# Optimization experiments

Hardware: AMD Instinct MI355X
Metric: run time of the kernel (lower is better)

## Reference

```python
import jax, jax.numpy as jnp
import numpy as np
from jax import lax

N = 100_000          # points
NEIGH = 16           # max_num_neighbors
E = N * NEIGH        # edges
DIN = 128            # num_inputs
D2 = 64              # bottleneck dim = num_outputs // 4
DOUT = 256           # num_outputs
K = 15               # num_kernel_points
SIGMA = 0.04         # kernel_influence_dist = prev_grid_size * sigma
NEG = 0.1            # LeakyReLU slope
EPS = 1e-5           # BatchNorm eps


def leaky(x):
    return jnp.where(x >= 0, x, NEG * x)


def batchnorm(x, g, b):
    # training-mode BN over the point dimension (biased variance, like torch)
    m = jnp.mean(x, axis=0)
    v = jnp.var(x, axis=0)
    return (x - m) * (g / jnp.sqrt(v + EPS)) + b


def setup_inputs() -> dict:
    key = jax.random.key(0)
    ks = jax.random.split(key, 12)
    pos = jax.random.uniform(ks[0], (N, 4), dtype=jnp.float32) * 0.1  # col 0: batch idx (unused, non-strided)
    x = jax.random.normal(ks[1], (N, DIN), dtype=jnp.float32)
    e_ref = jax.random.randint(ks[2], (E,), 0, N)
    e_query = jax.random.randint(ks[3], (E,), 0, N)
    # fixed kernel point positions within the influence radius
    kernel_points = jax.random.normal(ks[4], (K, 3), dtype=jnp.float32) * (0.5 * SIGMA)
    W1 = jax.random.normal(ks[5], (DIN, D2), dtype=jnp.float32) / np.sqrt(DIN)
    W_kp = jax.random.normal(ks[6], (K, D2, D2), dtype=jnp.float32) / np.sqrt(D2 * K)
    W2 = jax.random.normal(ks[7], (D2, DOUT), dtype=jnp.float32) / np.sqrt(D2)
    Wsc = jax.random.normal(ks[8], (DIN, DOUT), dtype=jnp.float32) / np.sqrt(DIN)
    ones = lambda d: jnp.ones((d,), jnp.float32)
    zeros = lambda d: jnp.zeros((d,), jnp.float32)
    return dict(pos=pos, x=x, e_ref=e_ref, e_query=e_query,
                W1=W1, g1=ones(D2), b1=zeros(D2),
                kernel_points=kernel_points, W_kp=W_kp, gkp=ones(D2), bkp=zeros(D2),
                W2=W2, g2=ones(DOUT), b2=zeros(DOUT),
                Wsc=Wsc, gsc=ones(DOUT), bsc=zeros(DOUT))


def reference(pos, x, e_ref, e_query, W1, g1, b1, kernel_points, W_kp, gkp, bkp,
              W2, g2, b2, Wsc, gsc, bsc):
    n = x.shape[0]
    # bottleneck unary_1: Linear(no bias) -> BN -> LeakyReLU
    h = leaky(batchnorm(x @ W1, g1, b1))                      # [N, D2]
    # KPConv (rigid, linear influence, 'sum' aggregation); non-strided: query_pos == pos
    rel = pos[e_ref, 1:] - pos[e_query, 1:]                    # [E, 3]
    d2 = jnp.sum((rel[:, None, :] - kernel_points[None]) ** 2, axis=-1)  # [E, K]
    infl = jnp.maximum(0.0, 1.0 - jnp.sqrt(d2) / SIGMA)        # [E, K]
    feat_e = h[e_ref]                                          # [E, D2] neighbor gather

    def body(acc, inp):
        infl_k, Wk = inp                                       # [E], [D2, D2]
        agg = jax.ops.segment_sum(infl_k[:, None] * feat_e, e_query, num_segments=n)
        return acc + agg @ Wk, None

    y0 = jnp.zeros((n, W_kp.shape[-1]), x.dtype)
    y, _ = lax.scan(body, y0, (infl.T, W_kp))                  # [N, D2]
    # SimpleBlock post: BN -> LeakyReLU
    y = leaky(batchnorm(y, gkp, bkp))
    # bottleneck unary_2: Linear -> BN -> LeakyReLU
    y = leaky(batchnorm(y @ W2, g2, b2))
    # shortcut (num_inputs != num_outputs): Linear -> BN, no activation; residual add
    skip = batchnorm(x @ Wsc, gsc, bsc)
    return y + skip
```

## Files before the change

### kernel.cpp

```cpp
#include <hip/hip_runtime.h>
#include <math.h>

#define NP   100000
#define EDG  1600000
#define NK   15
#define SIGK 0.04f
#define SCH  2048
#define SNB  49
#define MAXE 384
#define AGP  968

typedef __bf16 v8bf __attribute__((ext_vector_type(8)));
typedef __bf16 bf4  __attribute__((ext_vector_type(4)));
typedef float  v4f  __attribute__((ext_vector_type(4)));

__device__ __forceinline__ float lk(float v) { return v >= 0.f ? v : 0.1f * v; }
__device__ __forceinline__ float bf2f(__bf16 b) { return (float)b; }

template <int KIN, int NB, bool TRANS, bool OUTBF>
__global__ __launch_bounds__(256) void mgemm_k(const float* __restrict__ X,
                                               const __bf16* __restrict__ Wp,
                                               void* __restrict__ Out, int n, int Ntot,
                                               const float* __restrict__ ta,
                                               const float* __restrict__ tb,
                                               float* __restrict__ osum,
                                               float* __restrict__ osq) {
  constexpr int PITCH = KIN + 8;
  constexpr int NT = NB / 16;
  __shared__ __bf16 al[128 * PITCH];
  __shared__ float red[2][NB][4];
  const int tid = threadIdx.x;
  const int r0 = blockIdx.x << 7;
  const int nb0 = blockIdx.y * NB;

  constexpr int QKS = (KIN == 128) ? 5 : 4;
  for (int idx = tid; idx < (128 << QKS); idx += 256) {
    const int r = idx >> QKS, q = (idx & ((1 << QKS) - 1)) << 2;
    const int row = r0 + r;
    float4 v = make_float4(0.f, 0.f, 0.f, 0.f);
    if (row < n) {
      v = *(const float4*)&X[(size_t)row * KIN + q];
      if (TRANS) {
        v.x = lk(ta[q + 0] * v.x + tb[q + 0]);
        v.y = lk(ta[q + 1] * v.y + tb[q + 1]);
        v.z = lk(ta[q + 2] * v.z + tb[q + 2]);
        v.w = lk(ta[q + 3] * v.w + tb[q + 3]);
      }
    }
    bf4 o;
    o[0] = (__bf16)v.x; o[1] = (__bf16)v.y; o[2] = (__bf16)v.z; o[3] = (__bf16)v.w;
    *(bf4*)&al[r * PITCH + q] = o;
  }
  __syncthreads();

  const int wv = tid >> 6, lane = tid & 63;
  const int mr = lane & 15, quad = lane >> 4;
  const int ntg0 = nb0 >> 4;
  const int NTG = Ntot >> 4;
  v4f acc[2][NT];
#pragma unroll
  for (int a = 0; a < 2; ++a)
#pragma unroll
    for (int b = 0; b < NT; ++b) acc[a][b] = (v4f){0.f, 0.f, 0.f, 0.f};

#pragma unroll
  for (int ks = 0; ks < KIN / 32; ++ks) {
    v8bf bf[NT];
#pragma unroll
    for (int nt = 0; nt < NT; ++nt)
      bf[nt] = ((const v8bf*)Wp)[((size_t)ks * NTG + ntg0 + nt) * 64 + lane];
#pragma unroll
    for (int mt = 0; mt < 2; ++mt) {
      const int row = (wv << 5) + (mt << 4) + mr;
      const v8bf av = *(const v8bf*)&al[row * PITCH + (ks << 5) + (quad << 3)];
#pragma unroll
      for (int nt = 0; nt < NT; ++nt)
        acc[mt][nt] = __builtin_amdgcn_mfma_f32_16x16x32_bf16(av, bf[nt], acc[mt][nt], 0, 0, 0);
    }
  }

  float csum[NT], csq[NT];
#pragma unroll
  for (int nt = 0; nt < NT; ++nt) { csum[nt] = 0.f; csq[nt] = 0.f; }
#pragma unroll
  for (int mt = 0; mt < 2; ++mt)
#pragma unroll
    for (int nt = 0; nt < NT; ++nt)
#pragma unroll
      for (int r = 0; r < 4; ++r) {
        const float v = acc[mt][nt][r];
        const int row = r0 + (wv << 5) + (mt << 4) + (quad << 2) + r;
        if (row < n) {
          const size_t o = (size_t)row * Ntot + nb0 + (nt << 4) + mr;
          if (OUTBF) ((__bf16*)Out)[o] = (__bf16)v;
          else       ((float*)Out)[o] = v;
        }
        csum[nt] += v;
        csq[nt] += v * v;
      }
#pragma unroll
  for (int nt = 0; nt < NT; ++nt) {
    float s = csum[nt], q = csq[nt];
    s += __shfl_down(s, 32); s += __shfl_down(s, 16);
    q += __shfl_down(q, 32); q += __shfl_down(q, 16);
    if (quad == 0) { red[0][(nt << 4) + mr][wv] = s; red[1][(nt << 4) + mr][wv] = q; }
  }
  __syncthreads();
  if (tid < NB) {
    const float s = red[0][tid][0] + red[0][tid][1] + red[0][tid][2] + red[0][tid][3];
    const float q = red[1][tid][0] + red[1][tid][1] + red[1][tid][2] + red[1][tid][3];
    const int rep = (blockIdx.x & 31) * Ntot;
    atomicAdd(&osum[rep + nb0 + tid], s);
    atomicAdd(&osq[rep + nb0 + tid], q);
  }
}

__global__ void finalize_k(const float* __restrict__ sum, const float* __restrict__ sq,
                           const float* __restrict__ g, const float* __restrict__ b,
                           float* __restrict__ oa, float* __restrict__ ob, int C, int R,
                           float invn) {
  const int c = threadIdx.x;
  if (c < C) {
    float s = 0.f, q = 0.f;
    for (int r = 0; r < R; ++r) { s += sum[r * C + c]; q += sq[r * C + c]; }
    const float m = s * invn;
    const float var = q * invn - m * m;
    const float a = g[c] / sqrtf(var + 1e-5f);
    oa[c] = a;
    ob[c] = b[c] - m * a;
  }
}

__global__ __launch_bounds__(256) void normleaky_k(const __bf16* __restrict__ t,
                                                   __bf16* __restrict__ hb,
                                                   const float* __restrict__ a,
                                                   const float* __restrict__ b) {
  const int idx = (blockIdx.x << 8) + threadIdx.x;
  const int c = (idx << 2) & 63;
  const bf4 v = *(const bf4*)&t[(size_t)idx << 2];
  bf4 o;
  o[0] = (__bf16)lk(a[c + 0] * bf2f(v[0]) + b[c + 0]);
  o[1] = (__bf16)lk(a[c + 1] * bf2f(v[1]) + b[c + 1]);
  o[2] = (__bf16)lk(a[c + 2] * bf2f(v[2]) + b[c + 2]);
  o[3] = (__bf16)lk(a[c + 3] * bf2f(v[3]) + b[c + 3]);
  *(bf4*)&hb[(size_t)idx << 2] = o;
}

__global__ __launch_bounds__(256) void final_k(float* __restrict__ o,
                                               const __bf16* __restrict__ t2,
                                               const __bf16* __restrict__ tsc,
                                               const float* __restrict__ a2,
                                               const float* __restrict__ b2,
                                               const float* __restrict__ asc,
                                               const float* __restrict__ bsc) {
  const int idx = (blockIdx.x << 8) + threadIdx.x;
  const int c = (idx << 2) & 255;
  const bf4 tv = *(const bf4*)&t2[(size_t)idx << 2];
  const bf4 sv = *(const bf4*)&tsc[(size_t)idx << 2];
  float4 r;
  r.x = lk(a2[c + 0] * bf2f(tv[0]) + b2[c + 0]) + asc[c + 0] * bf2f(sv[0]) + bsc[c + 0];
  r.y = lk(a2[c + 1] * bf2f(tv[1]) + b2[c + 1]) + asc[c + 1] * bf2f(sv[1]) + bsc[c + 1];
  r.z = lk(a2[c + 2] * bf2f(tv[2]) + b2[c + 2]) + asc[c + 2] * bf2f(sv[2]) + bsc[c + 2];
  r.w = lk(a2[c + 3] * bf2f(tv[3]) + b2[c + 3]) + asc[c + 3] * bf2f(sv[3]) + bsc[c + 3];
  ((float4*)o)[idx] = r;
}

__device__ __forceinline__ bool edge_active(const float* __restrict__ pos,
                                            const float* __restrict__ kp,
                                            int ref, int q) {
  const float4 pr = *(const float4*)&pos[ref * 4];
  const float4 pq = *(const float4*)&pos[q * 4];
  const float rx = pr.y - pq.y, ry = pr.z - pq.z, rz = pr.w - pq.w;
  bool act = false;
#pragma unroll
  for (int k = 0; k < NK; ++k) {
    const float dx = rx - kp[k * 3 + 0];
    const float dy = ry - kp[k * 3 + 1];
    const float dz = rz - kp[k * 3 + 2];
    act = act || (dx * dx + dy * dy + dz * dz < SIGK * SIGK);
  }
  return act;
}

__global__ __launch_bounds__(256) void hist_k(const int* __restrict__ er,
                                              const int* __restrict__ eq,
                                              const float* __restrict__ pos,
                                              const float* __restrict__ kp,
                                              int* __restrict__ cnt,
                                              unsigned char* __restrict__ flags) {
  const int stride = gridDim.x << 8;
  for (int e = (blockIdx.x << 8) + threadIdx.x; e < EDG; e += stride) {
    const int q = eq[e];
    const bool act = edge_active(pos, kp, er[e], q);
    flags[e] = act ? 1 : 0;
    if (act) atomicAdd(&cnt[q], 1);
  }
}

__global__ __launch_bounds__(256) void scanA_k(const int* __restrict__ cnt, int* __restrict__ part) {
  __shared__ int s[256];
  const int tid = threadIdx.x;
  const int base = blockIdx.x * SCH;
  int acc = 0;
  for (int i = tid; i < SCH; i += 256) {
    const int idx = base + i;
    if (idx < NP) acc += cnt[idx];
  }
  s[tid] = acc;
  __syncthreads();
  for (int d = 128; d > 0; d >>= 1) {
    if (tid < d) s[tid] += s[tid + d];
    __syncthreads();
  }
  if (tid == 0) part[blockIdx.x] = s[0];
}

__global__ void scanB_k(int* __restrict__ part, int* __restrict__ off) {
  if (threadIdx.x == 0) {
    int run = 0;
    for (int i = 0; i < SNB; ++i) { const int v = part[i]; part[i] = run; run += v; }
    off[NP] = run;
  }
}

__global__ __launch_bounds__(256) void scanC_k(const int* __restrict__ cnt,
                                               const int* __restrict__ part,
                                               int* __restrict__ off, int* __restrict__ cur) {
  __shared__ int s[256];
  const int tid = threadIdx.x;
  const int base = blockIdx.x * SCH + tid * 8;
  int loc[8];
  int mysum = 0;
#pragma unroll
  for (int j = 0; j < 8; ++j) {
    const int idx = base + j;
    const int v = (idx < NP) ? cnt[idx] : 0;
    loc[j] = mysum;
    mysum += v;
  }
  s[tid] = mysum;
  __syncthreads();
  for (int d = 1; d < 256; d <<= 1) {
    int v = (tid >= d) ? s[tid - d] : 0;
    __syncthreads();
    s[tid] += v;
    __syncthreads();
  }
  const int tb = part[blockIdx.x] + s[tid] - mysum;
#pragma unroll
  for (int j = 0; j < 8; ++j) {
    const int idx = base + j;
    if (idx < NP) { off[idx] = tb + loc[j]; cur[idx] = tb + loc[j]; }
  }
}

__global__ __launch_bounds__(256) void scat_k(const int* __restrict__ er,
                                              const int* __restrict__ eq,
                                              const unsigned char* __restrict__ flags,
                                              int* __restrict__ cur, int* __restrict__ sref) {
  const int stride = gridDim.x << 8;
  for (int e = (blockIdx.x << 8) + threadIdx.x; e < EDG; e += stride) {
    if (flags[e]) {
      const int p = atomicAdd(&cur[eq[e]], 1);
      if (p < EDG) sref[p] = er[e];
    }
  }
}

__device__ __forceinline__ void wshuf1(const float* W, __bf16* Wp, int idx, int Ntot) {
  const int j = idx & 7;
  const int lane = (idx >> 3) & 63;
  const int rest = idx >> 9;
  const int NTG = Ntot >> 4;
  const int ntg = rest % NTG;
  const int ks = rest / NTG;
  Wp[idx] = (__bf16)W[(size_t)(ks * 32 + ((lane >> 4) << 3) + j) * Ntot + ntg * 16 + (lane & 15)];
}

__global__ __launch_bounds__(256) void allshuf_k(const float* __restrict__ W1,
                                                 const float* __restrict__ Wsc,
                                                 const float* __restrict__ W2,
                                                 const float* __restrict__ Wkp,
                                                 __bf16* __restrict__ base) {
  const int i = (blockIdx.x << 8) + threadIdx.x;
  if (i < 8192) {
    wshuf1(W1, base, i, 64);
  } else if (i < 40960) {
    wshuf1(Wsc, base + 8192, i - 8192, 256);
  } else if (i < 57344) {
    wshuf1(W2, base + 40960, i - 40960, 256);
  } else if (i < 118784) {
    const int idx = i - 57344;
    const int j = idx & 7;
    const int lane = (idx >> 3) & 63;
    const int nt = (idx >> 9) & 3;
    const int kb = (idx >> 11) & 1;
    const int k = idx >> 12;
    const int kd = kb * 32 + ((lane >> 4) << 3) + j;
    const int n = nt * 16 + (lane & 15);
    (base + 57344)[idx] = (__bf16)Wkp[(k * 64 + kd) * 64 + n];
  }
}

__global__ __launch_bounds__(256, 4) void kpagg_k(const float* __restrict__ pos,
                                                  const int* __restrict__ sref,
                                                  const int* __restrict__ off,
                                                  const float* __restrict__ kpts,
                                                  const __bf16* __restrict__ Wf,
                                                  const __bf16* __restrict__ hb,
                                                  float* __restrict__ y,
                                                  float* __restrict__ osum,
                                                  float* __restrict__ osq) {
  constexpr int INFL_BYTES = MAXE * 16 * 4;
  constexpr int UNION_BYTES = 16 * AGP * 2;
  __shared__ __align__(16) char uSm[UNION_BYTES];
  __shared__ int qoffL[17];
  __shared__ float kpL[48];
  float* inflF = (float*)uSm;
  int* refsL = (int*)(uSm + INFL_BYTES);
  __bf16* aggL = (__bf16*)uSm;

  const int tid = threadIdx.x;
  const int q0 = blockIdx.x << 4;
  if (tid < 17) qoffL[tid] = off[q0 + tid];
  if (tid >= 32 && tid < 32 + 45) kpL[tid - 32] = kpts[tid - 32];
  __syncthreads();

  const int e0 = qoffL[0];
  int nE = qoffL[16] - e0;
  if (nE > MAXE) nE = MAXE;
  if (nE == 0 && tid == 0) refsL[0] = 0;

  for (int i = tid; i < nE; i += 256) {
    const int e = e0 + i;
    const int ref = sref[e];
    refsL[i] = ref;
    int lo = 0, hi = 16;
    while (hi - lo > 1) { const int mid = (lo + hi) >> 1; if (qoffL[mid] <= e) lo = mid; else hi = mid; }
    const int q = q0 + lo;
    const float4 pr = *(const float4*)&pos[ref * 4];
    const float4 pq = *(const float4*)&pos[q * 4];
    const float rx = pr.y - pq.y, ry = pr.z - pq.z, rz = pr.w - pq.w;
    float wk[16];
#pragma unroll
    for (int k = 0; k < NK; ++k) {
      const float dx = rx - kpL[k * 3 + 0];
      const float dy = ry - kpL[k * 3 + 1];
      const float dz = rz - kpL[k * 3 + 2];
      const float w = 1.f - sqrtf(dx * dx + dy * dy + dz * dz) * (1.f / SIGK);
      wk[k] = w > 0.f ? w : 0.f;
    }
    wk[15] = 0.f;
    *(float4*)&inflF[i * 16 + 0]  = make_float4(wk[0], wk[1], wk[2], wk[3]);
    *(float4*)&inflF[i * 16 + 4]  = make_float4(wk[4], wk[5], wk[6], wk[7]);
    *(float4*)&inflF[i * 16 + 8]  = make_float4(wk[8], wk[9], wk[10], wk[11]);
    *(float4*)&inflF[i * 16 + 12] = make_float4(wk[12], wk[13], wk[14], wk[15]);
  }
  __syncthreads();

  const int wv = tid >> 6, lane = tid & 63;
  const int ql = (wv << 2) + (lane >> 4);
  const int t4 = (lane & 15) << 2;
  const int le0 = qoffL[ql] - e0;
  int le1 = qoffL[ql + 1] - e0;
  if (le1 > nE) le1 = nE;
  const int len = le1 - le0;

  float acc[NK][4];
#pragma unroll
  for (int k = 0; k < NK; ++k) { acc[k][0] = acc[k][1] = acc[k][2] = acc[k][3] = 0.f; }

  const int j0 = (len > 0) ? le0 : 0;
  const int j1 = (len > 1) ? le0 + 1 : j0;
  const int j2 = (len > 2) ? le0 + 2 : j1;
  bf4 hA = *(const bf4*)&hb[(size_t)refsL[j0] * 64 + t4];
  bf4 hB = *(const bf4*)&hb[(size_t)refsL[j1] * 64 + t4];
  int refC = refsL[j2];
#pragma unroll 1
  for (int j = le0; j < le1; ++j) {
    const bf4 hv = hA;
    hA = hB;
    hB = *(const bf4*)&hb[(size_t)refC * 64 + t4];
    const int jn = (j + 3 < le1) ? j + 3 : le1 - 1;
    refC = refsL[jn];
    const float f0 = bf2f(hv[0]), f1 = bf2f(hv[1]), f2 = bf2f(hv[2]), f3 = bf2f(hv[3]);
    const float4 wA = *(const float4*)&inflF[j * 16 + 0];
    const float4 wB = *(const float4*)&inflF[j * 16 + 4];
    const float4 wC = *(const float4*)&inflF[j * 16 + 8];
    const float4 wD = *(const float4*)&inflF[j * 16 + 12];
    const float wk[NK] = {wA.x, wA.y, wA.z, wA.w, wB.x, wB.y, wB.z, wB.w,
                          wC.x, wC.y, wC.z, wC.w, wD.x, wD.y, wD.z};
#pragma unroll
    for (int k = 0; k < NK; ++k) {
      acc[k][0] += wk[k] * f0;
      acc[k][1] += wk[k] * f1;
      acc[k][2] += wk[k] * f2;
      acc[k][3] += wk[k] * f3;
    }
  }

  __syncthreads();

#pragma unroll
  for (int k = 0; k < NK; ++k) {
    bf4 o;
    o[0] = (__bf16)acc[k][0]; o[1] = (__bf16)acc[k][1];
    o[2] = (__bf16)acc[k][2]; o[3] = (__bf16)acc[k][3];
    *(bf4*)&aggL[ql * AGP + k * 64 + t4] = o;
  }
  __syncthreads();

  const int m = lane & 15, quad = lane >> 4;
  v4f yacc = {0.f, 0.f, 0.f, 0.f};
  const v8bf* Wf8 = (const v8bf*)Wf;
#pragma unroll
  for (int k = 0; k < NK; ++k)
#pragma unroll
    for (int kb = 0; kb < 2; ++kb) {
      const v8bf av = *(const v8bf*)&aggL[m * AGP + k * 64 + kb * 32 + (quad << 3)];
      const v8bf bv = Wf8[((k * 2 + kb) * 4 + wv) * 64 + lane];
      yacc = __builtin_amdgcn_mfma_f32_16x16x32_bf16(av, bv, yacc, 0, 0, 0);
    }

  float s = 0.f, q2 = 0.f;
#pragma unroll
  for (int r = 0; r < 4; ++r) {
    const float v = yacc[r];
    y[(size_t)(q0 + (quad << 2) + r) * 64 + (wv << 4) + m] = v;
    s += v; q2 += v * v;
  }
  s += __shfl_down(s, 32); s += __shfl_down(s, 16);
  q2 += __shfl_down(q2, 32); q2 += __shfl_down(q2, 16);
  if (quad == 0) {
    const int rep = (blockIdx.x & 63) << 6;
    atomicAdd(&osum[rep + (wv << 4) + m], s);
    atomicAdd(&osq[rep + (wv << 4) + m], q2);
  }
}

extern "C" void kernel_launch(void* const* d_in, const int* in_sizes, int n_in,
                              void* d_out, int out_size, void* d_ws, size_t ws_size,
                              hipStream_t stream) {
  const float* pos = (const float*)d_in[0];
  const float* x   = (const float*)d_in[1];
  const int* er    = (const int*)d_in[2];
  const int* eq    = (const int*)d_in[3];
  const float* W1  = (const float*)d_in[4];
  const float* g1  = (const float*)d_in[5];
  const float* b1  = (const float*)d_in[6];
  const float* kp  = (const float*)d_in[7];
  const float* Wkp = (const float*)d_in[8];
  const float* gkp = (const float*)d_in[9];
  const float* bkp = (const float*)d_in[10];
  const float* W2  = (const float*)d_in[11];
  const float* g2  = (const float*)d_in[12];
  const float* b2  = (const float*)d_in[13];
  const float* Wsc = (const float*)d_in[14];
  const float* gsc = (const float*)d_in[15];
  const float* bsc = (const float*)d_in[16];
  float* out = (float*)d_out;
  float* ws = (float*)d_ws;

  float* sum1 = ws;
  float* sq1  = ws + 2048;
  float* sumsc = ws + 4096;
  float* sqsc  = ws + 12288;
  float* sumy = ws + 20480;
  float* sqy  = ws + 24576;
  float* sum2 = ws + 28672;
  float* sq2  = ws + 36864;
  float* a1v = ws + 45056;   float* b1v  = ws + 45120;
  float* ascv = ws + 45184;  float* bscv = ws + 45440;
  float* ayv = ws + 45696;   float* byv  = ws + 45760;
  float* a2v = ws + 45824;   float* b2v  = ws + 46080;

  __bf16* Wpb = (__bf16*)(ws + 49152);
  __bf16* W1p = Wpb;
  __bf16* Wscp = Wpb + 8192;
  __bf16* W2p = Wpb + 40960;
  __bf16* Wfp = Wpb + 57344;
  __bf16* hb = (__bf16*)(ws + 114688);
  float* ybuf = ws + 114688 + 3200000;
  float* t1bf = ybuf + 6400000;
  __bf16* t1b = (__bf16*)t1bf;
  __bf16* tscb = (__bf16*)ybuf;
  int* cnt = (int*)(t1bf + 6400000);
  int* off = cnt + 100352;
  int* cur = off + 100352;
  int* part = cur + 100352;
  int* sref = part + 256;
  unsigned char* flags = (unsigned char*)(sref + EDG);
  __bf16* t2b = (__bf16*)cnt;

  const float invn = 1.f / (float)NP;

  (void)hipMemsetAsync(ws, 0, 49152 * sizeof(float), stream);
  (void)hipMemsetAsync(cnt, 0, 100352 * sizeof(int), stream);

  allshuf_k<<<464, 256, 0, stream>>>(W1, Wsc, W2, Wkp, Wpb);

  mgemm_k<128, 64, false, true><<<dim3(782, 1), 256, 0, stream>>>(
      x, W1p, t1b, NP, 64, nullptr, nullptr, sum1, sq1);
  finalize_k<<<1, 256, 0, stream>>>(sum1, sq1, g1, b1, a1v, b1v, 64, 32, invn);
  normleaky_k<<<6250, 256, 0, stream>>>(t1b, hb, a1v, b1v);

  hist_k<<<2048, 256, 0, stream>>>(er, eq, pos, kp, cnt, flags);
  scanA_k<<<SNB, 256, 0, stream>>>(cnt, part);
  scanB_k<<<1, 64, 0, stream>>>(part, off);
  scanC_k<<<SNB, 256, 0, stream>>>(cnt, part, off, cur);
  scat_k<<<2048, 256, 0, stream>>>(er, eq, flags, cur, sref);

  kpagg_k<<<6250, 256, 0, stream>>>(pos, sref, off, kp, Wfp, hb, ybuf, sumy, sqy);
  finalize_k<<<1, 256, 0, stream>>>(sumy, sqy, gkp, bkp, ayv, byv, 64, 64, invn);

  mgemm_k<64, 128, true, true><<<dim3(782, 2), 256, 0, stream>>>(
      ybuf, W2p, t2b, NP, 256, ayv, byv, sum2, sq2);
  finalize_k<<<1, 256, 0, stream>>>(sum2, sq2, g2, b2, a2v, b2v, 256, 32, invn);

  mgemm_k<128, 128, false, true><<<dim3(782, 2), 256, 0, stream>>>(
      x, Wscp, tscb, NP, 256, nullptr, nullptr, sumsc, sqsc);
  finalize_k<<<1, 256, 0, stream>>>(sumsc, sqsc, gsc, bsc, ascv, bscv, 256, 32, invn);

  final_k<<<25000, 256, 0, stream>>>(out, t2b, tscb, a2v, b2v, ascv, bscv);
}
```

Baseline: 519.0 us.

## Fuse BN+LeakyReLU of bottleneck into KPConv aggregation and simplify edge setup

Removes the separate normleaky pass and instead applies the first BatchNorm affine plus LeakyReLU on the fly to each gathered bf16 row inside kpagg_k. This saves a full write and read of the hidden feature buffer and one launch, at the cost of recomputing the activation for every edge gather. The edge setup also changes: it precomputes a per-edge query index table and caches query positions in shared memory instead of a binary search and a global load. It pads the influence stride to reduce LDS bank conflicts, lowers MAXE to 256 with one edge per thread, and unrolls the main loop by two. Lowering MAXE relies on the filtered per-block edge count staying under 256.

```diff
diff --git a/kernel.cpp b/kernel.cpp
--- a/kernel.cpp
+++ b/kernel.cpp
@@ -7,8 +7,9 @@
 #define SIGK 0.04f
 #define SCH  2048
 #define SNB  49
-#define MAXE 384
+#define MAXE 256
 #define AGP  968
+#define ISTR 20
 
 typedef __bf16 v8bf __attribute__((ext_vector_type(8)));
 typedef __bf16 bf4  __attribute__((ext_vector_type(4)));
@@ -129,21 +130,6 @@
     oa[c] = a;
     ob[c] = b[c] - m * a;
   }
-}
-
-__global__ __launch_bounds__(256) void normleaky_k(const __bf16* __restrict__ t,
-                                                   __bf16* __restrict__ hb,
-                                                   const float* __restrict__ a,
-                                                   const float* __restrict__ b) {
-  const int idx = (blockIdx.x << 8) + threadIdx.x;
-  const int c = (idx << 2) & 63;
-  const bf4 v = *(const bf4*)&t[(size_t)idx << 2];
-  bf4 o;
-  o[0] = (__bf16)lk(a[c + 0] * bf2f(v[0]) + b[c + 0]);
-  o[1] = (__bf16)lk(a[c + 1] * bf2f(v[1]) + b[c + 1]);
-  o[2] = (__bf16)lk(a[c + 2] * bf2f(v[2]) + b[c + 2]);
-  o[3] = (__bf16)lk(a[c + 3] * bf2f(v[3]) + b[c + 3]);
-  *(bf4*)&hb[(size_t)idx << 2] = o;
 }
 
 __global__ __launch_bounds__(256) void final_k(float* __restrict__ o,
@@ -307,15 +293,19 @@
                                                   const int* __restrict__ off,
                                                   const float* __restrict__ kpts,
                                                   const __bf16* __restrict__ Wf,
-                                                  const __bf16* __restrict__ hb,
+                                                  const __bf16* __restrict__ t1b,
+                                                  const float* __restrict__ av,
+                                                  const float* __restrict__ bv,
                                                   float* __restrict__ y,
                                                   float* __restrict__ osum,
                                                   float* __restrict__ osq) {
-  constexpr int INFL_BYTES = MAXE * 16 * 4;
+  constexpr int INFL_BYTES = MAXE * ISTR * 4;
   constexpr int UNION_BYTES = 16 * AGP * 2;
   __shared__ __align__(16) char uSm[UNION_BYTES];
   __shared__ int qoffL[17];
   __shared__ float kpL[48];
+  __shared__ float4 qposL[16];
+  __shared__ unsigned char qidxL[MAXE];
   float* inflF = (float*)uSm;
   int* refsL = (int*)(uSm + INFL_BYTES);
   __bf16* aggL = (__bf16*)uSm;
@@ -323,7 +313,8 @@
   const int tid = threadIdx.x;
   const int q0 = blockIdx.x << 4;
   if (tid < 17) qoffL[tid] = off[q0 + tid];
-  if (tid >= 32 && tid < 32 + 45) kpL[tid - 32] = kpts[tid - 32];
+  if (tid >= 32 && tid < 77) kpL[tid - 32] = kpts[tid - 32];
+  if (tid >= 80 && tid < 96) qposL[tid - 80] = *(const float4*)&pos[(q0 + tid - 80) * 4];
   __syncthreads();
 
   const int e0 = qoffL[0];
@@ -331,15 +322,20 @@
   if (nE > MAXE) nE = MAXE;
   if (nE == 0 && tid == 0) refsL[0] = 0;
 
-  for (int i = tid; i < nE; i += 256) {
-    const int e = e0 + i;
-    const int ref = sref[e];
+  if (tid < 16) {
+    int a = qoffL[tid] - e0, b = qoffL[tid + 1] - e0;
+    if (a > nE) a = nE;
+    if (b > nE) b = nE;
+    for (int i = a; i < b; ++i) qidxL[i] = (unsigned char)tid;
+  }
+  __syncthreads();
+
+  if (tid < nE) {
+    const int i = tid;
+    const int ref = sref[e0 + i];
     refsL[i] = ref;
-    int lo = 0, hi = 16;
-    while (hi - lo > 1) { const int mid = (lo + hi) >> 1; if (qoffL[mid] <= e) lo = mid; else hi = mid; }
-    const int q = q0 + lo;
     const float4 pr = *(const float4*)&pos[ref * 4];
-    const float4 pq = *(const float4*)&pos[q * 4];
+    const float4 pq = qposL[qidxL[i]];
     const float rx = pr.y - pq.y, ry = pr.z - pq.z, rz = pr.w - pq.w;
     float wk[16];
 #pragma unroll
@@ -351,10 +347,10 @@
       wk[k] = w > 0.f ? w : 0.f;
     }
     wk[15] = 0.f;
-    *(float4*)&inflF[i * 16 + 0]  = make_float4(wk[0], wk[1], wk[2], wk[3]);
-    *(float4*)&inflF[i * 16 + 4]  = make_float4(wk[4], wk[5], wk[6], wk[7]);
-    *(float4*)&inflF[i * 16 + 8]  = make_float4(wk[8], wk[9], wk[10], wk[11]);
-    *(float4*)&inflF[i * 16 + 12] = make_float4(wk[12], wk[13], wk[14], wk[15]);
+    *(float4*)&inflF[i * ISTR + 0]  = make_float4(wk[0], wk[1], wk[2], wk[3]);
+    *(float4*)&inflF[i * ISTR + 4]  = make_float4(wk[4], wk[5], wk[6], wk[7]);
+    *(float4*)&inflF[i * ISTR + 8]  = make_float4(wk[8], wk[9], wk[10], wk[11]);
+    *(float4*)&inflF[i * ISTR + 12] = make_float4(wk[12], wk[13], wk[14], wk[15]);
   }
   __syncthreads();
 
@@ -366,6 +362,9 @@
   if (le1 > nE) le1 = nE;
   const int len = le1 - le0;
 
+  const float4 aV = *(const float4*)&av[t4];
+  const float4 bV = *(const float4*)&bv[t4];
+
   float acc[NK][4];
 #pragma unroll
   for (int k = 0; k < NK; ++k) { acc[k][0] = acc[k][1] = acc[k][2] = acc[k][3] = 0.f; }
@@ -373,21 +372,24 @@
   const int j0 = (len > 0) ? le0 : 0;
   const int j1 = (len > 1) ? le0 + 1 : j0;
   const int j2 = (len > 2) ? le0 + 2 : j1;
-  bf4 hA = *(const bf4*)&hb[(size_t)refsL[j0] * 64 + t4];
-  bf4 hB = *(const bf4*)&hb[(size_t)refsL[j1] * 64 + t4];
+  bf4 hA = *(const bf4*)&t1b[(size_t)refsL[j0] * 64 + t4];
+  bf4 hB = *(const bf4*)&t1b[(size_t)refsL[j1] * 64 + t4];
   int refC = refsL[j2];
-#pragma unroll 1
+#pragma unroll 2
   for (int j = le0; j < le1; ++j) {
     const bf4 hv = hA;
     hA = hB;
-    hB = *(const bf4*)&hb[(size_t)refC * 64 + t4];
+    hB = *(const bf4*)&t1b[(size_t)refC * 64 + t4];
     const int jn = (j + 3 < le1) ? j + 3 : le1 - 1;
     refC = refsL[jn];
-    const float f0 = bf2f(hv[0]), f1 = bf2f(hv[1]), f2 = bf2f(hv[2]), f3 = bf2f(hv[3]);
-    const float4 wA = *(const float4*)&inflF[j * 16 + 0];
-    const float4 wB = *(const float4*)&inflF[j * 16 + 4];
-    const float4 wC = *(const float4*)&inflF[j * 16 + 8];
-    const float4 wD = *(const float4*)&inflF[j * 16 + 12];
+    const float f0 = lk(aV.x * bf2f(hv[0]) + bV.x);
+    const float f1 = lk(aV.y * bf2f(hv[1]) + bV.y);
+    const float f2 = lk(aV.z * bf2f(hv[2]) + bV.z);
+    const float f3 = lk(aV.w * bf2f(hv[3]) + bV.w);
+    const float4 wA = *(const float4*)&inflF[j * ISTR + 0];
+    const float4 wB = *(const float4*)&inflF[j * ISTR + 4];
+    const float4 wC = *(const float4*)&inflF[j * ISTR + 8];
+    const float4 wD = *(const float4*)&inflF[j * ISTR + 12];
     const float wk[NK] = {wA.x, wA.y, wA.z, wA.w, wB.x, wB.y, wB.z, wB.w,
                           wC.x, wC.y, wC.z, wC.w, wD.x, wD.y, wD.z};
 #pragma unroll
@@ -417,9 +419,9 @@
   for (int k = 0; k < NK; ++k)
 #pragma unroll
     for (int kb = 0; kb < 2; ++kb) {
-      const v8bf av = *(const v8bf*)&aggL[m * AGP + k * 64 + kb * 32 + (quad << 3)];
-      const v8bf bv = Wf8[((k * 2 + kb) * 4 + wv) * 64 + lane];
-      yacc = __builtin_amdgcn_mfma_f32_16x16x32_bf16(av, bv, yacc, 0, 0, 0);
+      const v8bf av2 = *(const v8bf*)&aggL[m * AGP + k * 64 + kb * 32 + (quad << 3)];
+      const v8bf bv2 = Wf8[((k * 2 + kb) * 4 + wv) * 64 + lane];
+      yacc = __builtin_amdgcn_mfma_f32_16x16x32_bf16(av2, bv2, yacc, 0, 0, 0);
     }
 
   float s = 0.f, q2 = 0.f;
@@ -479,7 +481,6 @@
   __bf16* Wscp = Wpb + 8192;
   __bf16* W2p = Wpb + 40960;
   __bf16* Wfp = Wpb + 57344;
-  __bf16* hb = (__bf16*)(ws + 114688);
   float* ybuf = ws + 114688 + 3200000;
   float* t1bf = ybuf + 6400000;
   __bf16* t1b = (__bf16*)t1bf;
@@ -502,7 +503,6 @@
   mgemm_k<128, 64, false, true><<<dim3(782, 1), 256, 0, stream>>>(
       x, W1p, t1b, NP, 64, nullptr, nullptr, sum1, sq1);
   finalize_k<<<1, 256, 0, stream>>>(sum1, sq1, g1, b1, a1v, b1v, 64, 32, invn);
-  normleaky_k<<<6250, 256, 0, stream>>>(t1b, hb, a1v, b1v);
 
   hist_k<<<2048, 256, 0, stream>>>(er, eq, pos, kp, cnt, flags);
   scanA_k<<<SNB, 256, 0, stream>>>(cnt, part);
@@ -510,7 +510,8 @@
   scanC_k<<<SNB, 256, 0, stream>>>(cnt, part, off, cur);
   scat_k<<<2048, 256, 0, stream>>>(er, eq, flags, cur, sref);
 
-  kpagg_k<<<6250, 256, 0, stream>>>(pos, sref, off, kp, Wfp, hb, ybuf, sumy, sqy);
+  kpagg_k<<<6250, 256, 0, stream>>>(pos, sref, off, kp, Wfp, t1b, a1v, b1v,
+                                    ybuf, sumy, sqy);
   finalize_k<<<1, 256, 0, stream>>>(sumy, sqy, gkp, bkp, ayv, byv, 64, 64, invn);
 
   mgemm_k<64, 128, true, true><<<dim3(782, 2), 256, 0, stream>>>(
```

After: 526.2 us. No clear change (+1.4%).
